# Kernel optimization log

Measured on AMD Instinct MI355X. Metric: run time of the kernel, lower is better.

The kernel has to match this reference:

```python
import jax, jax.numpy as jnp
import numpy as np

GRID = 256          # grid_size
PAD = 30            # padding_size
GLOBAL = GRID + 2 * PAD   # 316
OUT = 512           # deform_input_size
K = 2 * PAD + 1     # 61 Gaussian kernel


def make_gaussian(size=K, a=1.0, b=0.5, fwhm1=100.0, fwhm2=25.0):
    x = np.arange(size, dtype=np.float64)
    c = size // 2
    r2 = (x[None, :] - c) ** 2 + (x[:, None] - c) ** 2
    g1 = np.exp(-4.0 * np.log(2.0) * r2 / fwhm1 ** 2)
    g2 = np.exp(-4.0 * np.log(2.0) * r2 / fwhm2 ** 2)
    return (a * g1 - b * g2).astype(np.float32)


def p_basis():
    # P[0,i,j] = (j - PAD)/(GRID-1) ; P[1,i,j] = (i - PAD)/(GRID-1)
    coord = (jnp.arange(GLOBAL, dtype=jnp.float32) - PAD) / (GRID - 1.0)
    px = jnp.broadcast_to(coord[None, :], (GLOBAL, GLOBAL))
    py = jnp.broadcast_to(coord[:, None], (GLOBAL, GLOBAL))
    return jnp.stack([px, py], axis=0)  # [2, 316, 316]


def base_grid():
    lin = jnp.linspace(-1.0, 1.0, OUT, dtype=jnp.float32)
    w = jnp.broadcast_to(lin[None, :], (OUT, OUT))  # x varies along columns
    h = jnp.broadcast_to(lin[:, None], (OUT, OUT))  # y varies along rows
    return jnp.stack([w, h], axis=-1)  # [512, 512, 2]


def grid_sample_bilinear(img, grid):
    """F.grid_sample, mode=bilinear, padding_mode=zeros, align_corners=True.
    img: [B,C,H,W], grid: [B,Hg,Wg,2] with (x,y) in [-1,1]."""
    B, C, H, W = img.shape
    gx = (grid[..., 0] + 1.0) * (W - 1) * 0.5
    gy = (grid[..., 1] + 1.0) * (H - 1) * 0.5
    x0 = jnp.floor(gx); y0 = jnp.floor(gy)
    wx1 = gx - x0; wx0 = 1.0 - wx1
    wy1 = gy - y0; wy0 = 1.0 - wy1

    def gather(ix, iy):
        valid = ((ix >= 0) & (ix <= W - 1) & (iy >= 0) & (iy <= H - 1)).astype(img.dtype)
        ixc = jnp.clip(ix, 0, W - 1).astype(jnp.int32)
        iyc = jnp.clip(iy, 0, H - 1).astype(jnp.int32)
        v = jax.vmap(lambda im, yy, xx: im[:, yy, xx])(img, iyc, ixc)  # [B,C,Hg,Wg]
        return v * valid[:, None]

    out = (gather(x0, y0) * (wx0 * wy0)[:, None]
           + gather(x0 + 1, y0) * (wx1 * wy0)[:, None]
           + gather(x0, y0 + 1) * (wx0 * wy1)[:, None]
           + gather(x0 + 1, y0 + 1) * (wx1 * wy1)[:, None])
    return out


def setup_inputs() -> dict:
    key = jax.random.key(0)
    k1, k2 = jax.random.split(key)
    x = jax.random.normal(k1, (8, 32, 512, 512), dtype=jnp.float32)
    xs = jax.random.uniform(k2, (8, 1, 256, 256), dtype=jnp.float32)
    gauss_kernel = jnp.asarray(make_gaussian())  # [61,61] fixed conv weight
    return {"x": x, "xs": xs, "gauss_kernel": gauss_kernel}


def reference(x, xs, gauss_kernel):
    B = xs.shape[0]
    xs = xs.reshape(B, 1, GRID, GRID)
    # ReplicationPad2d(PAD)
    xs_hm = jnp.pad(xs, ((0, 0), (0, 0), (PAD, PAD), (PAD, PAD)), mode="edge")  # [B,1,316,316]
    P = p_basis()  # [2,316,316]
    # channel 0: xs_hm (-> p_filter); channels 1,2: P * xs (-> x/y numerators)
    stacked = jnp.concatenate([xs_hm, P[None] * xs_hm], axis=1)  # [B,3,316,316]
    inp = stacked.reshape(B * 3, 1, GLOBAL, GLOBAL)
    kern = gauss_kernel.reshape(1, 1, K, K)
    conv = jax.lax.conv_general_dilated(inp, kern, (1, 1), "VALID")  # [B*3,1,256,256]
    conv = conv.reshape(B, 3, GRID, GRID)
    p_f = conv[:, 0]
    x_f = conv[:, 1] / p_f
    y_f = conv[:, 2] / p_f
    xg = jnp.clip(x_f * 2.0 - 1.0, -1.0, 1.0)
    yg = jnp.clip(y_f * 2.0 - 1.0, -1.0, 1.0)
    grid = jnp.stack([xg, yg], axis=1)  # [B,2,256,256]
    # nn.Upsample bilinear (align_corners=False) == jax.image.resize half-pixel bilinear
    grid_up = jax.image.resize(grid, (B, 2, OUT, OUT), method="bilinear")
    grid_l = jnp.transpose(grid_up, (0, 2, 3, 1))  # [B,512,512,2]
    grid_r = (49.0 * base_grid()[None] + grid_l) / 50.0
    x_sampled = grid_sample_bilinear(x, grid_r)  # [B,C,512,512]
    return x_sampled, grid_up
```

## Files before the change

### kernel.cpp

```cpp
#include <hip/hip_runtime.h>
#include <math.h>

#define GRID_N 256
#define PADN   30
#define GLOB_N 316
#define KS     61
#define OUT_N  512
#define BATCH  8
#define CHAN   32
#define CPB    8

#define STH    4
#define SSR    8
#define SCOLS  512
#define SLOTS  1024
#define BUFS   4160

typedef float v2f __attribute__((ext_vector_type(2)));

#define GLD16(gaddr, laddr)                                                       \
    __builtin_amdgcn_global_load_lds(                                             \
        (const __attribute__((address_space(1))) void*)(gaddr),                   \
        (__attribute__((address_space(3))) void*)(laddr), 16, 0, 0)

__device__ __forceinline__ void compute_weights(float* w1, float* w2) {
    int t = threadIdx.x;
    if (t < KS) {
        double d  = (double)(t - PADN);
        double r2 = d * d;
        const double c = 2.772588722239781;
        w1[t] = (float)exp(-c * r2 / 10000.0);
        w2[t] = (float)exp(-c * r2 / 625.0);
    }
}

__global__ __launch_bounds__(256) void hpass_kernel(const float* __restrict__ xs,
                                                    float* __restrict__ H) {
    __shared__ float srow[GLOB_N];
    __shared__ float w1[KS], w2[KS];
    int b  = blockIdx.x / GLOB_N;
    int gi = blockIdx.x % GLOB_N;
    int t  = threadIdx.x;

    compute_weights(w1, w2);

    int iy = gi - PADN;
    iy = iy < 0 ? 0 : (iy > GRID_N - 1 ? GRID_N - 1 : iy);
    const float* src = xs + ((size_t)b * GRID_N + iy) * GRID_N;
    for (int j = t; j < GLOB_N; j += 256) {
        int ix = j - PADN;
        ix = ix < 0 ? 0 : (ix > GRID_N - 1 ? GRID_N - 1 : ix);
        srow[j] = src[ix];
    }
    __syncthreads();

    float a1 = 0.f, a2 = 0.f, a3 = 0.f, a4 = 0.f;
    for (int v = 0; v < KS; ++v) {
        float s  = srow[t + v];
        float cc = (float)(t + v - PADN) * (1.0f / 255.0f);
        float cs = cc * s;
        float cw1 = w1[v], cw2 = w2[v];
        a1 += cw1 * s;
        a2 += cw2 * s;
        a3 += cw1 * cs;
        a4 += cw2 * cs;
    }
    size_t cst  = (size_t)GLOB_N * GRID_N;
    size_t base = ((size_t)(b * 4) * GLOB_N + gi) * GRID_N + t;
    H[base]           = a1;
    H[base + cst]     = a2;
    H[base + 2 * cst] = a3;
    H[base + 3 * cst] = a4;
}

__global__ __launch_bounds__(256) void vpass_kernel(const float* __restrict__ H,
                                                    float* __restrict__ g256) {
    __shared__ float w1[KS], w2[KS];
    int bid = (int)blockIdx.x;
    bid = (bid & 7) * 256 + (bid >> 3);
    int b = bid >> 8;
    int y = bid & 255;
    int t = threadIdx.x;

    compute_weights(w1, w2);
    __syncthreads();

    const float* Hb = H + (size_t)b * 4 * GLOB_N * GRID_N;
    size_t cst = (size_t)GLOB_N * GRID_N;

    float s1 = 0.f, s2 = 0.f, sx1 = 0.f, sx2 = 0.f, sy1 = 0.f, sy2 = 0.f;
    for (int u = 0; u < KS; ++u) {
        size_t off = (size_t)(y + u) * GRID_N + t;
        float h1 = Hb[off];
        float h2 = Hb[off + cst];
        float h3 = Hb[off + 2 * cst];
        float h4 = Hb[off + 3 * cst];
        float cw1 = w1[u], cw2 = w2[u];
        float cc = (float)(y + u - PADN) * (1.0f / 255.0f);
        s1  += cw1 * h1;
        s2  += cw2 * h2;
        sx1 += cw1 * h3;
        sx2 += cw2 * h4;
        sy1 += cw1 * (cc * h1);
        sy2 += cw2 * (cc * h2);
    }
    float p  = s1 - 0.5f * s2;
    float xf = (sx1 - 0.5f * sx2) / p;
    float yf = (sy1 - 0.5f * sy2) / p;
    float xg = fminf(fmaxf(xf * 2.0f - 1.0f, -1.0f), 1.0f);
    float yg = fminf(fmaxf(yf * 2.0f - 1.0f, -1.0f), 1.0f);

    size_t o = (size_t)(b * 2) * GRID_N * GRID_N + (size_t)y * GRID_N + t;
    g256[o] = xg;
    g256[o + (size_t)GRID_N * GRID_N] = yg;
}

__global__ __launch_bounds__(256) void upsample_kernel(const float* __restrict__ g256,
                                                       float* __restrict__ gup) {
    int idx = blockIdx.x * 256 + threadIdx.x;
    int ox = idx & (OUT_N - 1);
    int oy = (idx >> 9) & (OUT_N - 1);
    int b  = idx >> 18;

    float sx = 0.5f * (float)ox - 0.25f;
    float sy = 0.5f * (float)oy - 0.25f;
    float fxf = floorf(sx), fyf = floorf(sy);
    int x0 = (int)fxf, y0 = (int)fyf;
    float fx = sx - fxf, fy = sy - fyf;
    int x0c = x0 < 0 ? 0 : x0;
    int x1c = x0 + 1 > GRID_N - 1 ? GRID_N - 1 : x0 + 1;
    int y0c = y0 < 0 ? 0 : y0;
    int y1c = y0 + 1 > GRID_N - 1 ? GRID_N - 1 : y0 + 1;

    for (int c = 0; c < 2; ++c) {
        const float* g = g256 + ((size_t)(b * 2 + c)) * GRID_N * GRID_N;
        float v00 = g[y0c * GRID_N + x0c];
        float v10 = g[y0c * GRID_N + x1c];
        float v01 = g[y1c * GRID_N + x0c];
        float v11 = g[y1c * GRID_N + x1c];
        float v = (v00 * (1.f - fx) + v10 * fx) * (1.f - fy)
                + (v01 * (1.f - fx) + v11 * fx) * fy;
        gup[((size_t)(b * 2 + c)) * OUT_N * OUT_N + (size_t)oy * OUT_N + ox] = v;
    }
}

__global__ __launch_bounds__(256) void sample_kernel(const float* __restrict__ x,
                                                     const float* __restrict__ gup,
                                                     float* __restrict__ out) {
    __shared__ float tile[2 * BUFS];

    int bid = (int)blockIdx.x;
    bid = (bid & 7) * 512 + (bid >> 3);
    int b  = bid >> 9;
    int cg = (bid >> 7) & 3;
    int rg = bid & 127;
    int ty = rg * STH;
    int c0 = cg * CPB;

    int t  = threadIdx.x;
    int r  = t >> 6;
    int cb = (t & 63) * 2;

    int goff[4];
    {
        int baserow = ty - 2 + (t >> 7);
        int scol = (t & 127) * 4;
        #pragma unroll
        for (int k = 0; k < 4; ++k) {
            int rr = baserow + 2 * k;
            rr = rr < 0 ? 0 : (rr > OUT_N - 1 ? OUT_N - 1 : rr);
            goff[k] = rr * OUT_N + scol;
        }
    }
    int wb0 = (t & ~63);

    float w00[8], w10[8], w01[8], w11[8];
    int lbase[8];
    int oy = ty + r;
    {
        size_t gplane = (size_t)OUT_N * OUT_N;
        size_t grow = (size_t)(b * 2) * gplane + (size_t)oy * OUT_N;
        float by = -1.0f + (float)oy * (2.0f / 511.0f);
        #pragma unroll
        for (int k = 0; k < 4; ++k) {
            #pragma unroll
            for (int h = 0; h < 2; ++h) {
                int j = k * 2 + h;
                int ox = 128 * k + cb + h;
                float gxu = gup[grow + ox];
                float gyu = gup[grow + ox + gplane];
                float bx = -1.0f + (float)ox * (2.0f / 511.0f);
                float gx = (49.0f * bx + gxu) * 0.02f;
                float gy = (49.0f * by + gyu) * 0.02f;
                float pxf = (gx + 1.0f) * 255.5f;
                float pyf = (gy + 1.0f) * 255.5f;
                float fx0 = floorf(pxf), fy0 = floorf(pyf);
                int x0 = (int)fx0, y0 = (int)fy0;
                float fx = pxf - fx0, fy = pyf - fy0;
                w00[j] = (1.f - fx) * (1.f - fy);
                w10[j] = fx * (1.f - fy);
                w01[j] = (1.f - fx) * fy;
                w11[j] = fx * fy;
                lbase[j] = (y0 - (ty - 2)) * SCOLS + x0;
            }
        }
    }

    size_t plane = (size_t)OUT_N * OUT_N;
    const float* xb = x + ((size_t)b * CHAN + c0) * plane;
    float* ob = out + ((size_t)b * CHAN + c0) * plane;
    size_t orow = (size_t)oy * OUT_N;

    #define STAGE(c, bufIdx)                                                     \
        do {                                                                     \
            const float* xc_ = xb + (size_t)(c) * plane;                         \
            _Pragma("unroll")                                                    \
            for (int k_ = 0; k_ < 4; ++k_)                                       \
                GLD16(xc_ + goff[k_],                                            \
                      &tile[(bufIdx) * BUFS + (k_ * 256 + wb0) * 4]);            \
        } while (0)

    STAGE(0, 0);
    STAGE(1, 1);

    for (int c = 0; c < CPB; ++c) {
        if (c == 0 || c == CPB - 1) asm volatile("s_waitcnt vmcnt(4)" ::: "memory");
        else                        asm volatile("s_waitcnt vmcnt(8)" ::: "memory");
        __builtin_amdgcn_s_barrier();
        __builtin_amdgcn_sched_barrier(0);

        const float* tb_ = &tile[(c & 1) * BUFS];
        float* oc = ob + (size_t)c * plane;
        #pragma unroll
        for (int k = 0; k < 4; ++k) {
            float vv0, vv1;
            {
                int j = k * 2;
                int lb = lbase[j];
                vv0 = w00[j] * tb_[lb] + w10[j] * tb_[lb + 1]
                    + w01[j] * tb_[lb + SCOLS] + w11[j] * tb_[lb + SCOLS + 1];
            }
            {
                int j = k * 2 + 1;
                int lb = lbase[j];
                vv1 = w00[j] * tb_[lb] + w10[j] * tb_[lb + 1]
                    + w01[j] * tb_[lb + SCOLS] + w11[j] * tb_[lb + SCOLS + 1];
            }
            v2f st; st.x = vv0; st.y = vv1;
            __builtin_nontemporal_store(st, (v2f*)(oc + orow + cb + 128 * k));
        }

        __builtin_amdgcn_sched_barrier(0);
        __builtin_amdgcn_s_barrier();
        __builtin_amdgcn_sched_barrier(0);

        if (c + 2 < CPB) STAGE(c + 2, c & 1);
    }
    #undef STAGE
}

extern "C" void kernel_launch(void* const* d_in, const int* in_sizes, int n_in,
                              void* d_out, int out_size, void* d_ws, size_t ws_size,
                              hipStream_t stream) {
    (void)in_sizes; (void)n_in; (void)d_ws; (void)ws_size; (void)out_size;
    const float* x  = (const float*)d_in[0];
    const float* xs = (const float*)d_in[1];

    float* out = (float*)d_out;
    const size_t XS_OUT = (size_t)BATCH * CHAN * OUT_N * OUT_N;
    float* gup = out + XS_OUT;

    float* H    = out;
    float* g256 = out + 4u * 1024 * 1024;

    hipLaunchKernelGGL(hpass_kernel, dim3(BATCH * GLOB_N), dim3(256), 0, stream, xs, H);
    hipLaunchKernelGGL(vpass_kernel, dim3(BATCH * GRID_N), dim3(256), 0, stream, H, g256);
    hipLaunchKernelGGL(upsample_kernel, dim3(BATCH * OUT_N * OUT_N / 256), dim3(256), 0, stream,
                       g256, gup);
    const int SBLOCKS = BATCH * (CHAN / CPB) * (OUT_N / STH);
    hipLaunchKernelGGL(sample_kernel, dim3(SBLOCKS), dim3(256), 0, stream, x, gup, out);
}
```

Baseline: 138.9 us.

## Triple-buffer sample kernel LDS staging and register-block vertical pass over four rows

The sample kernel moves from double to triple LDS buffering. The next prefetch is issued right after the wait barrier, which drops the second per-channel barrier and lets loads overlap compute longer. The vertical conv pass now computes four output rows per thread so each loaded H value is reused across rows, cutting global loads and block count. The cost is more LDS per block (three buffers, padding removed), which may lower occupancy, and more registers in the vpass.

```diff
diff --git a/kernel.cpp b/kernel.cpp
--- a/kernel.cpp
+++ b/kernel.cpp
@@ -13,8 +13,7 @@
 #define STH    4
 #define SSR    8
 #define SCOLS  512
-#define SLOTS  1024
-#define BUFS   4160
+#define BUFS   4096
 
 typedef float v2f __attribute__((ext_vector_type(2)));
 
@@ -77,9 +76,9 @@
                                                     float* __restrict__ g256) {
     __shared__ float w1[KS], w2[KS];
     int bid = (int)blockIdx.x;
-    bid = (bid & 7) * 256 + (bid >> 3);
-    int b = bid >> 8;
-    int y = bid & 255;
+    bid = (bid & 7) * 64 + (bid >> 3);
+    int b  = bid >> 6;
+    int y0 = (bid & 63) * 4;
     int t = threadIdx.x;
 
     compute_weights(w1, w2);
@@ -88,31 +87,43 @@
     const float* Hb = H + (size_t)b * 4 * GLOB_N * GRID_N;
     size_t cst = (size_t)GLOB_N * GRID_N;
 
-    float s1 = 0.f, s2 = 0.f, sx1 = 0.f, sx2 = 0.f, sy1 = 0.f, sy2 = 0.f;
-    for (int u = 0; u < KS; ++u) {
-        size_t off = (size_t)(y + u) * GRID_N + t;
+    float s1[4], s2[4], sx1[4], sx2[4], sy1[4], sy2[4];
+    #pragma unroll
+    for (int dy = 0; dy < 4; ++dy) {
+        s1[dy] = s2[dy] = sx1[dy] = sx2[dy] = sy1[dy] = sy2[dy] = 0.f;
+    }
+
+    for (int u = 0; u < KS + 3; ++u) {
+        size_t off = (size_t)(y0 + u) * GRID_N + t;
         float h1 = Hb[off];
         float h2 = Hb[off + cst];
         float h3 = Hb[off + 2 * cst];
         float h4 = Hb[off + 3 * cst];
-        float cw1 = w1[u], cw2 = w2[u];
-        float cc = (float)(y + u - PADN) * (1.0f / 255.0f);
-        s1  += cw1 * h1;
-        s2  += cw2 * h2;
-        sx1 += cw1 * h3;
-        sx2 += cw2 * h4;
-        sy1 += cw1 * (cc * h1);
-        sy2 += cw2 * (cc * h2);
-    }
-    float p  = s1 - 0.5f * s2;
-    float xf = (sx1 - 0.5f * sx2) / p;
-    float yf = (sy1 - 0.5f * sy2) / p;
-    float xg = fminf(fmaxf(xf * 2.0f - 1.0f, -1.0f), 1.0f);
-    float yg = fminf(fmaxf(yf * 2.0f - 1.0f, -1.0f), 1.0f);
-
-    size_t o = (size_t)(b * 2) * GRID_N * GRID_N + (size_t)y * GRID_N + t;
-    g256[o] = xg;
-    g256[o + (size_t)GRID_N * GRID_N] = yg;
+        float cc = (float)(y0 + u - PADN) * (1.0f / 255.0f);
+        float ch1 = cc * h1, ch2 = cc * h2;
+        #pragma unroll
+        for (int dy = 0; dy < 4; ++dy) {
+            int k = u - dy;
+            if (k >= 0 && k < KS) {
+                float a = w1[k], bw = w2[k];
+                s1[dy]  += a * h1;  s2[dy]  += bw * h2;
+                sx1[dy] += a * h3;  sx2[dy] += bw * h4;
+                sy1[dy] += a * ch1; sy2[dy] += bw * ch2;
+            }
+        }
+    }
+
+    #pragma unroll
+    for (int dy = 0; dy < 4; ++dy) {
+        float p  = s1[dy] - 0.5f * s2[dy];
+        float xf = (sx1[dy] - 0.5f * sx2[dy]) / p;
+        float yf = (sy1[dy] - 0.5f * sy2[dy]) / p;
+        float xg = fminf(fmaxf(xf * 2.0f - 1.0f, -1.0f), 1.0f);
+        float yg = fminf(fmaxf(yf * 2.0f - 1.0f, -1.0f), 1.0f);
+        size_t o = (size_t)(b * 2) * GRID_N * GRID_N + (size_t)(y0 + dy) * GRID_N + t;
+        g256[o] = xg;
+        g256[o + (size_t)GRID_N * GRID_N] = yg;
+    }
 }
 
 __global__ __launch_bounds__(256) void upsample_kernel(const float* __restrict__ g256,
@@ -147,7 +158,7 @@
 __global__ __launch_bounds__(256) void sample_kernel(const float* __restrict__ x,
                                                      const float* __restrict__ gup,
                                                      float* __restrict__ out) {
-    __shared__ float tile[2 * BUFS];
+    __shared__ float tile[3 * BUFS];
 
     int bid = (int)blockIdx.x;
     bid = (bid & 7) * 512 + (bid >> 3);
@@ -211,25 +222,28 @@
     float* ob = out + ((size_t)b * CHAN + c0) * plane;
     size_t orow = (size_t)oy * OUT_N;
 
-    #define STAGE(c, bufIdx)                                                     \
+    #define STAGE(c)                                                             \
         do {                                                                     \
             const float* xc_ = xb + (size_t)(c) * plane;                         \
+            float* lb_ = &tile[((c) % 3) * BUFS];                                \
             _Pragma("unroll")                                                    \
             for (int k_ = 0; k_ < 4; ++k_)                                       \
-                GLD16(xc_ + goff[k_],                                            \
-                      &tile[(bufIdx) * BUFS + (k_ * 256 + wb0) * 4]);            \
+                GLD16(xc_ + goff[k_], lb_ + (k_ * 256 + wb0) * 4);               \
         } while (0)
 
-    STAGE(0, 0);
-    STAGE(1, 1);
+    STAGE(0);
+    STAGE(1);
 
     for (int c = 0; c < CPB; ++c) {
-        if (c == 0 || c == CPB - 1) asm volatile("s_waitcnt vmcnt(4)" ::: "memory");
-        else                        asm volatile("s_waitcnt vmcnt(8)" ::: "memory");
+        if (c == 0)                 asm volatile("s_waitcnt vmcnt(4)" ::: "memory");
+        else if (c == 1 || c == CPB - 1) asm volatile("s_waitcnt vmcnt(8)" ::: "memory");
+        else                        asm volatile("s_waitcnt vmcnt(12)" ::: "memory");
         __builtin_amdgcn_s_barrier();
         __builtin_amdgcn_sched_barrier(0);
 
-        const float* tb_ = &tile[(c & 1) * BUFS];
+        if (c + 2 < CPB) STAGE(c + 2);
+
+        const float* tb_ = &tile[(c % 3) * BUFS];
         float* oc = ob + (size_t)c * plane;
         #pragma unroll
         for (int k = 0; k < 4; ++k) {
@@ -249,12 +263,7 @@
             v2f st; st.x = vv0; st.y = vv1;
             __builtin_nontemporal_store(st, (v2f*)(oc + orow + cb + 128 * k));
         }
-
         __builtin_amdgcn_sched_barrier(0);
-        __builtin_amdgcn_s_barrier();
-        __builtin_amdgcn_sched_barrier(0);
-
-        if (c + 2 < CPB) STAGE(c + 2, c & 1);
     }
     #undef STAGE
 }
@@ -274,7 +283,7 @@
     float* g256 = out + 4u * 1024 * 1024;
 
     hipLaunchKernelGGL(hpass_kernel, dim3(BATCH * GLOB_N), dim3(256), 0, stream, xs, H);
-    hipLaunchKernelGGL(vpass_kernel, dim3(BATCH * GRID_N), dim3(256), 0, stream, H, g256);
+    hipLaunchKernelGGL(vpass_kernel, dim3(BATCH * GRID_N / 4), dim3(256), 0, stream, H, g256);
     hipLaunchKernelGGL(upsample_kernel, dim3(BATCH * OUT_N * OUT_N / 256), dim3(256), 0, stream,
                        g256, gup);
     const int SBLOCKS = BATCH * (CHAN / CPB) * (OUT_N / STH);
```

New measurement: 149.4 us. 7.6% more time.
